# Optimization experiments

Measured on AMD Instinct MI355X. Metric: run time of the kernel, lower is better.

## Reference

```python
import jax, jax.numpy as jnp
import numpy as np

HIDDEN = 4096
N_HEADS = 32
QK_NOPE = 128
QK_ROPE = 64
QK_HEAD = QK_NOPE + QK_ROPE  # 192
V_HEAD = 128
Q_LORA = 1536
KV_LORA = 512
EPS = 1e-6
ROPE_BASE = 10000.0
T = 2048


def rmsnorm(x, g, eps=EPS):
    var = jnp.mean(x * x, axis=-1, keepdims=True)
    return x * jax.lax.rsqrt(var + eps) * g


def apply_rope_interleaved(x, cos, sin):
    # non-neox style: rotate interleaved pairs. x: [T, ..., d]; cos/sin: [T, d//2]
    x1 = x[..., 0::2]
    x2 = x[..., 1::2]
    while cos.ndim < x1.ndim:
        cos = cos[:, None]
        sin = sin[:, None]
    o1 = x1 * cos - x2 * sin
    o2 = x1 * sin + x2 * cos
    return jnp.stack([o1, o2], axis=-1).reshape(x.shape)


def setup_inputs() -> dict:
    key = jax.random.key(0)
    ks = jax.random.split(key, 8)
    s = lambda fan_in: 1.0 / np.sqrt(fan_in)
    return {
        "positions": jnp.arange(T, dtype=jnp.int32),
        "hidden_states": jax.random.normal(ks[0], (T, HIDDEN), jnp.float32),
        "wq_a": jax.random.normal(ks[1], (HIDDEN, Q_LORA), jnp.float32) * s(HIDDEN),
        "gq": jnp.ones((Q_LORA,), jnp.float32),
        "wq_b": jax.random.normal(ks[2], (Q_LORA, N_HEADS * QK_HEAD), jnp.float32) * s(Q_LORA),
        "wkv_a": jax.random.normal(ks[3], (HIDDEN, KV_LORA + QK_ROPE), jnp.float32) * s(HIDDEN),
        "gkv": jnp.ones((KV_LORA,), jnp.float32),
        "wkv_b": jax.random.normal(ks[4], (KV_LORA, N_HEADS * (QK_NOPE + V_HEAD)), jnp.float32) * s(KV_LORA),
        "wo": jax.random.normal(ks[5], (N_HEADS * V_HEAD, HIDDEN), jnp.float32) * s(N_HEADS * V_HEAD),
    }


def reference(positions, hidden_states, wq_a, gq, wq_b, wkv_a, gkv, wkv_b, wo):
    t = hidden_states.shape[0]
    scale = QK_HEAD ** -0.5

    # Q path: low-rank down-proj -> RMSNorm -> up-proj
    q = rmsnorm(hidden_states @ wq_a, gq) @ wq_b  # [T, H*192]
    q = q.reshape(t, N_HEADS, QK_HEAD)
    q_nope, q_pe = q[..., :QK_NOPE], q[..., QK_NOPE:]

    # KV path: compressed latent + decoupled rope key
    kv_a = hidden_states @ wkv_a  # [T, kv_lora + rope]
    c_kv, k_pe = kv_a[:, :KV_LORA], kv_a[:, KV_LORA:]
    kv = rmsnorm(c_kv, gkv) @ wkv_b  # [T, H*(nope+v)]
    kv = kv.reshape(t, N_HEADS, QK_NOPE + V_HEAD)
    k_nope, v = kv[..., :QK_NOPE], kv[..., QK_NOPE:]

    # RoPE (interleaved / non-neox)
    inv_freq = 1.0 / (ROPE_BASE ** (jnp.arange(0, QK_ROPE, 2, dtype=jnp.float32) / QK_ROPE))
    angles = positions.astype(jnp.float32)[:, None] * inv_freq[None, :]  # [T, rope/2]
    cos, sin = jnp.cos(angles), jnp.sin(angles)
    q_pe = apply_rope_interleaved(q_pe, cos, sin)          # [T, H, rope]
    k_pe = apply_rope_interleaved(k_pe, cos, sin)          # [T, rope]

    q_full = jnp.concatenate([q_nope, q_pe], axis=-1)       # [T, H, 192]
    k_full = jnp.concatenate(
        [k_nope, jnp.broadcast_to(k_pe[:, None, :], (t, N_HEADS, QK_ROPE))], axis=-1)

    scores = jnp.einsum('qhd,khd->hqk', q_full, k_full) * scale  # [H, T, T]
    causal = positions[:, None] >= positions[None, :]
    scores = jnp.where(causal[None], scores, jnp.finfo(scores.dtype).min)
    probs = jax.nn.softmax(scores, axis=-1)
    attn = jnp.einsum('hqk,khd->qhd', probs, v)              # [T, H, 128]
    return attn.reshape(t, N_HEADS * V_HEAD) @ wo            # [T, hidden]
```

## Files before the change

kernel.cpp:

```cpp
#include <hip/hip_runtime.h>
#include <hip/hip_bf16.h>
#include <stdint.h>

typedef __hip_bfloat16 bf16;
typedef unsigned short u16;
typedef short v8s __attribute__((ext_vector_type(8)));
typedef float v4f __attribute__((ext_vector_type(4)));

#define T_LEN   2048
#define HIDDEN  4096
#define N_HEADS 32
#define QK_NOPE 128
#define QK_ROPE 64
#define QK_HEAD 192
#define V_HEAD  128
#define Q_LORA  1536
#define KV_LORA 512
#define NFUSE   2176

enum { DT_BF16 = 0, DT_F32 = 1, DT_EXT = 2 };

__device__ __forceinline__ u16 f2b(float x) {
    union { bf16 h; u16 u; } cv; cv.h = __float2bfloat16(x); return cv.u;
}

typedef const __attribute__((address_space(1))) uint32_t* gas_ptr;
typedef __attribute__((address_space(3))) uint32_t* las_ptr;
__device__ __forceinline__ void gll16(const void* g, void* l) {
    __builtin_amdgcn_global_load_lds((gas_ptr)g, (las_ptr)l, 16, 0, 0);
}

__global__ __launch_bounds__(256) void convert_bf16(
    const void* __restrict__ X, u16* __restrict__ Y, int nelem,
    const uint32_t* __restrict__ probe)
{
    const bool f32 = (probe[0] & 0xFFFFu) == 0u;
    const int i = (blockIdx.x * 256 + threadIdx.x) * 8;
    if (i >= nelem) return;
    if (f32) {
        const float* x = (const float*)X + i;
        u16 o[8];
        #pragma unroll
        for (int e = 0; e < 8; ++e) o[e] = f2b(x[e]);
        *(uint4*)(Y + i) = *(const uint4*)o;
    } else {
        *(uint4*)(Y + i) = *(const uint4*)((const u16*)X + i);
    }
}

__global__ __launch_bounds__(256) void transpose_to_bf16(
    const void* __restrict__ W, u16* __restrict__ Wt,
    int K, int N, const uint32_t* __restrict__ probe)
{
    const bool f32 = (probe[0] & 0xFFFFu) == 0u;
    __shared__ uint32_t Ts[64 * 33];
    const int n0 = blockIdx.x * 64;
    const int k0 = blockIdx.y * 64;
    const int tid = threadIdx.x;
    {
        const int nc = (tid & 7) * 8;
        const int kp = tid >> 3;
        const int k = k0 + kp * 2;
        uint32_t vals[8];
        if (n0 >= N) {
            #pragma unroll
            for (int e = 0; e < 8; ++e) vals[e] = 0;
        } else if (f32) {
            const float* w0 = (const float*)W + (size_t)k * N + n0 + nc;
            const float* w1 = w0 + N;
            #pragma unroll
            for (int e = 0; e < 8; ++e)
                vals[e] = (uint32_t)f2b(w0[e]) | ((uint32_t)f2b(w1[e]) << 16);
        } else {
            const u16* w0 = (const u16*)W + (size_t)k * N + n0 + nc;
            const u16* w1 = w0 + N;
            u16 a[8], b[8];
            *(uint4*)a = *(const uint4*)w0;
            *(uint4*)b = *(const uint4*)w1;
            #pragma unroll
            for (int e = 0; e < 8; ++e)
                vals[e] = (uint32_t)a[e] | ((uint32_t)b[e] << 16);
        }
        #pragma unroll
        for (int e = 0; e < 8; ++e)
            Ts[(nc + e) * 33 + kp] = vals[e];
    }
    __syncthreads();
    {
        const int n = tid >> 2;
        const int kp0 = (tid & 3) * 8;
        u16 out[16];
        #pragma unroll
        for (int j = 0; j < 8; ++j) {
            const uint32_t v = Ts[n * 33 + kp0 + j];
            out[2 * j]     = (u16)(v & 0xFFFFu);
            out[2 * j + 1] = (u16)(v >> 16);
        }
        u16* dst = Wt + (size_t)(n0 + n) * K + k0 + kp0 * 2;
        *(uint4*)dst = *(const uint4*)out;
        *(uint4*)(dst + 8) = *(const uint4*)(out + 8);
    }
}

__global__ __launch_bounds__(256) void gemm_bt(
    const u16* __restrict__ A, const u16* __restrict__ Bt,
    void* __restrict__ C, int ccode,
    int N, int K, const uint32_t* __restrict__ probe)
{
    __shared__ __align__(16) u16 As[128 * 32];
    __shared__ __align__(16) u16 Bs[128 * 32];

    const int tid  = threadIdx.x;
    const int lane = tid & 63;
    const int wave = tid >> 6;
    const int quad = lane >> 4, l15 = lane & 15;
    const int wr = (wave >> 1) * 64, wc = (wave & 1) * 64;

    const int gx  = gridDim.x;
    const int nwg = gx * gridDim.y;
    int bid = blockIdx.y * gx + blockIdx.x;
    if ((nwg & 7) == 0)
        bid = (bid & 7) * (nwg >> 3) + (bid >> 3);
    const int bxl = bid % gx;
    const int byl = bid / gx;
    const size_t brow = (size_t)byl * 128;
    const size_t bcol = (size_t)bxl * 128;

    v4f acc[4][4];
    #pragma unroll
    for (int i = 0; i < 4; ++i)
        #pragma unroll
        for (int j = 0; j < 4; ++j)
            acc[i][j] = (v4f){0.f, 0.f, 0.f, 0.f};

    const int c0 = tid, c1 = tid + 256;
    const int r0 = c0 >> 2, e0 = (c0 & 3) * 8;
    const int r1 = c1 >> 2, e1 = (c1 & 3) * 8;
    const u16* Ab = A + brow * K;
    const u16* Bb = Bt + bcol * K;

    for (int k0 = 0; k0 < K; k0 += 32) {
        gll16(Ab + (size_t)r0 * K + k0 + e0, (void*)(As + c0 * 8));
        gll16(Ab + (size_t)r1 * K + k0 + e1, (void*)(As + c1 * 8));
        gll16(Bb + (size_t)r0 * K + k0 + e0, (void*)(Bs + c0 * 8));
        gll16(Bb + (size_t)r1 * K + k0 + e1, (void*)(Bs + c1 * 8));
        __syncthreads();

        v8s af[4], bf[4];
        #pragma unroll
        for (int i = 0; i < 4; ++i)
            af[i] = *(const v8s*)(As + (wr + i * 16 + l15) * 32 + quad * 8);
        #pragma unroll
        for (int j = 0; j < 4; ++j)
            bf[j] = *(const v8s*)(Bs + (wc + j * 16 + l15) * 32 + quad * 8);
        #pragma unroll
        for (int i = 0; i < 4; ++i)
            #pragma unroll
            for (int j = 0; j < 4; ++j)
                acc[i][j] = __builtin_amdgcn_mfma_f32_16x16x32_bf16(
                    af[i], bf[j], acc[i][j], 0, 0, 0);
        __syncthreads();
    }

    const bool c_f32 = (ccode == DT_F32) ||
                       (ccode == DT_EXT && (probe[0] & 0xFFFFu) == 0u);
    #pragma unroll
    for (int i = 0; i < 4; ++i) {
        #pragma unroll
        for (int r = 0; r < 4; ++r) {
            const size_t row = brow + wr + i * 16 + quad * 4 + r;
            #pragma unroll
            for (int j = 0; j < 4; ++j) {
                const size_t col = bcol + wc + j * 16 + l15;
                if (c_f32) ((float*)C)[row * N + col] = acc[i][j][r];
                else       ((u16*)C)[row * N + col]   = f2b(acc[i][j][r]);
            }
        }
    }
}

__global__ __launch_bounds__(256) void rmsnorm_kernel(
    const float* __restrict__ x, const void* __restrict__ g,
    bf16* __restrict__ y, int cols,
    const uint32_t* __restrict__ probe)
{
    const bool g_f32 = (probe[0] & 0xFFFFu) == 0u;
    const int row = blockIdx.x;
    const float* xr = x + (size_t)row * NFUSE;
    float ss = 0.f;
    for (int c = threadIdx.x; c < cols; c += 256) {
        float v = xr[c];
        ss += v * v;
    }
    #pragma unroll
    for (int off = 32; off > 0; off >>= 1) ss += __shfl_down(ss, off, 64);
    __shared__ float wsum[4];
    const int wave = threadIdx.x >> 6, lane = threadIdx.x & 63;
    if (lane == 0) wsum[wave] = ss;
    __syncthreads();
    const float tot = wsum[0] + wsum[1] + wsum[2] + wsum[3];
    const float inv = rsqrtf(tot / (float)cols + 1e-6f);
    for (int c = threadIdx.x; c < cols; c += 256) {
        const float gv = g_f32 ? ((const float*)g)[c]
                               : __bfloat162float(((const bf16*)g)[c]);
        y[(size_t)row * cols + c] = __float2bfloat16(xr[c] * inv * gv);
    }
}

__global__ void kpe_rope_kernel(const float* __restrict__ qkv,
                                const int* __restrict__ pos,
                                bf16* __restrict__ kpe)
{
    const int t = blockIdx.x;
    const int i = threadIdx.x;
    const float x1 = qkv[(size_t)t * NFUSE + 2048 + 2 * i];
    const float x2 = qkv[(size_t)t * NFUSE + 2048 + 2 * i + 1];
    const float inv_freq = powf(10000.f, -(float)(2 * i) / 64.f);
    const float ang = (float)pos[t] * inv_freq;
    float s, c;
    sincosf(ang, &s, &c);
    kpe[(size_t)t * 64 + 2 * i]     = __float2bfloat16(x1 * c - x2 * s);
    kpe[(size_t)t * 64 + 2 * i + 1] = __float2bfloat16(x1 * s + x2 * c);
}

__global__ __launch_bounds__(256) void qpe_rope_kernel(bf16* __restrict__ q,
                                                       const int* __restrict__ pos)
{
    const int idx = blockIdx.x * 256 + threadIdx.x;
    const int i = idx & 31;
    const int h = (idx >> 5) & 31;
    const int t = idx >> 10;
    if (t >= T_LEN) return;
    bf16* base = q + ((size_t)t * N_HEADS + h) * QK_HEAD + QK_NOPE + 2 * i;
    const float x1 = __bfloat162float(base[0]);
    const float x2 = __bfloat162float(base[1]);
    const float inv_freq = powf(10000.f, -(float)(2 * i) / 64.f);
    const float ang = (float)pos[t] * inv_freq;
    float s, c;
    sincosf(ang, &s, &c);
    base[0] = __float2bfloat16(x1 * c - x2 * s);
    base[1] = __float2bfloat16(x1 * s + x2 * c);
}

#define KS_LD 200
#define VT_LD 72
#define PS_LD 72

__global__ __launch_bounds__(256) void attn_mfma(
    const bf16* __restrict__ qg, const bf16* __restrict__ kvg,
    const bf16* __restrict__ kpeg, bf16* __restrict__ attng)
{
    __shared__ u16 Ks[64 * KS_LD];
    __shared__ u16 Vt[V_HEAD * VT_LD];
    __shared__ u16 Ps[4 * 32 * PS_LD];

    const int bx = blockIdx.x;
    const int h  = bx & 31;
    const int g  = bx >> 5;
    const int qt = (bx < 256) ? (15 - g) : (g - 8);
    const int q0 = qt * 128;
    const int nkt = 2 * qt + 2;

    const int tid  = threadIdx.x;
    const int wave = tid >> 6, lane = tid & 63;
    const int quad = lane >> 4, l15 = lane & 15;
    const float scale = 0.07216878364870323f;

    v8s qf[2][6];
    #pragma unroll
    for (int mi = 0; mi < 2; ++mi)
        #pragma unroll
        for (int ks = 0; ks < 6; ++ks)
            qf[mi][ks] = *(const v8s*)((const u16*)qg +
                (size_t)(q0 + wave * 32 + mi * 16 + l15) * 6144 +
                h * 192 + ks * 32 + quad * 8);

    v4f accO[2][8];
    #pragma unroll
    for (int mi = 0; mi < 2; ++mi)
        #pragma unroll
        for (int vs = 0; vs < 8; ++vs)
            accO[mi][vs] = (v4f){0.f, 0.f, 0.f, 0.f};
    float m_run[2][4], l_run[2][4];
    #pragma unroll
    for (int mi = 0; mi < 2; ++mi)
        #pragma unroll
        for (int r = 0; r < 4; ++r) { m_run[mi][r] = -1e30f; l_run[mi][r] = 0.f; }

    for (int kt = 0; kt < nkt; ++kt) {
        const int k0 = kt * 64;
        __syncthreads();
        {
            const int jj = tid >> 4;
            const int c0 = (tid & 15) * 16;
            #pragma unroll
            for (int p = 0; p < 4; ++p) {
                const int j = jj + p * 16;
                const u16* src = (const u16*)kvg +
                    (size_t)(k0 + j) * 8192 + h * 256 + c0;
                uint4 v0 = *(const uint4*)src;
                uint4 v1 = *(const uint4*)(src + 8);
                if (c0 < 128) {
                    u16* dst = &Ks[j * KS_LD + c0];
                    *(uint4*)dst = v0;
                    *(uint4*)(dst + 8) = v1;
                } else {
                    u16 buf[16];
                    *(uint4*)buf = v0;
                    *(uint4*)(buf + 8) = v1;
                    const int d0 = c0 - 128;
                    #pragma unroll
                    for (int e = 0; e < 16; ++e) {
                        const int d = d0 + e;
                        const int jswz = j ^ (((d >> 4) & 7) << 3);
                        Vt[d * VT_LD + jswz] = buf[e];
                    }
                }
            }
            const int j2 = tid >> 2;
            const int c2 = (tid & 3) * 16;
            const u16* src = (const u16*)kpeg + (size_t)(k0 + j2) * 64 + c2;
            uint4 w0 = *(const uint4*)src;
            uint4 w1 = *(const uint4*)(src + 8);
            u16* dst = &Ks[j2 * KS_LD + 128 + c2];
            *(uint4*)dst = w0;
            *(uint4*)(dst + 8) = w1;
        }
        __syncthreads();

        v4f accS[2][4];
        #pragma unroll
        for (int mi = 0; mi < 2; ++mi)
            #pragma unroll
            for (int nj = 0; nj < 4; ++nj)
                accS[mi][nj] = (v4f){0.f, 0.f, 0.f, 0.f};
        #pragma unroll
        for (int ks = 0; ks < 6; ++ks) {
            v8s kf[4];
            #pragma unroll
            for (int nj = 0; nj < 4; ++nj)
                kf[nj] = *(const v8s*)&Ks[(nj * 16 + l15) * KS_LD + ks * 32 + quad * 8];
            #pragma unroll
            for (int mi = 0; mi < 2; ++mi)
                #pragma unroll
                for (int nj = 0; nj < 4; ++nj)
                    accS[mi][nj] = __builtin_amdgcn_mfma_f32_16x16x32_bf16(
                        qf[mi][ks], kf[nj], accS[mi][nj], 0, 0, 0);
        }

        const bool need_mask = (kt >= 2 * qt);
        float p[2][4][4];
        float alpha[2][4];
        #pragma unroll
        for (int mi = 0; mi < 2; ++mi) {
            #pragma unroll
            for (int r = 0; r < 4; ++r) {
                const int qrow = q0 + wave * 32 + mi * 16 + quad * 4 + r;
                float sv[4];
                float rm = -1e30f;
                #pragma unroll
                for (int nj = 0; nj < 4; ++nj) {
                    float s = accS[mi][nj][r] * scale;
                    if (need_mask) {
                        const int jgl = k0 + nj * 16 + l15;
                        if (jgl > qrow) s = -1e30f;
                    }
                    sv[nj] = s;
                    rm = fmaxf(rm, s);
                }
                rm = fmaxf(rm, __shfl_xor(rm, 1));
                rm = fmaxf(rm, __shfl_xor(rm, 2));
                rm = fmaxf(rm, __shfl_xor(rm, 4));
                rm = fmaxf(rm, __shfl_xor(rm, 8));
                const float mo = m_run[mi][r];
                const float mn = fmaxf(mo, rm);
                const float al = __expf(mo - mn);
                float ps = 0.f;
                #pragma unroll
                for (int nj = 0; nj < 4; ++nj) {
                    const float pv = __expf(sv[nj] - mn);
                    p[mi][nj][r] = pv;
                    ps += pv;
                }
                ps += __shfl_xor(ps, 1);
                ps += __shfl_xor(ps, 2);
                ps += __shfl_xor(ps, 4);
                ps += __shfl_xor(ps, 8);
                l_run[mi][r] = l_run[mi][r] * al + ps;
                m_run[mi][r] = mn;
                alpha[mi][r] = al;
            }
        }

        #pragma unroll
        for (int mi = 0; mi < 2; ++mi)
            #pragma unroll
            for (int vs = 0; vs < 8; ++vs)
                #pragma unroll
                for (int r = 0; r < 4; ++r)
                    accO[mi][vs][r] *= alpha[mi][r];

        u16* psw = &Ps[wave * 32 * PS_LD];
        #pragma unroll
        for (int mi = 0; mi < 2; ++mi)
            #pragma unroll
            for (int nj = 0; nj < 4; ++nj)
                #pragma unroll
                for (int r = 0; r < 4; ++r)
                    psw[(mi * 16 + quad * 4 + r) * PS_LD + nj * 16 + l15] =
                        f2b(p[mi][nj][r]);

        #pragma unroll
        for (int kf = 0; kf < 2; ++kf) {
            v8s pf[2];
            #pragma unroll
            for (int mi = 0; mi < 2; ++mi)
                pf[mi] = *(const v8s*)&psw[(mi * 16 + l15) * PS_LD + kf * 32 + quad * 8];
            #pragma unroll
            for (int vs = 0; vs < 8; ++vs) {
                const int swz = (vs & 7) << 3;
                v8s vf = *(const v8s*)&Vt[(vs * 16 + l15) * VT_LD +
                                          ((kf * 32 + quad * 8) ^ swz)];
                #pragma unroll
                for (int mi = 0; mi < 2; ++mi)
                    accO[mi][vs] = __builtin_amdgcn_mfma_f32_16x16x32_bf16(
                        pf[mi], vf, accO[mi][vs], 0, 0, 0);
            }
        }
    }

    #pragma unroll
    for (int mi = 0; mi < 2; ++mi) {
        #pragma unroll
        for (int r = 0; r < 4; ++r) {
            const int qrow = q0 + wave * 32 + mi * 16 + quad * 4 + r;
            const float linv = 1.f / l_run[mi][r];
            #pragma unroll
            for (int vs = 0; vs < 8; ++vs)
                attng[(size_t)qrow * 4096 + h * 128 + vs * 16 + l15] =
                    __float2bfloat16(accO[mi][vs][r] * linv);
        }
    }
}

extern "C" void kernel_launch(void* const* d_in, const int* in_sizes, int n_in,
                              void* d_out, int out_size, void* d_ws, size_t ws_size,
                              hipStream_t stream)
{
    const int*  pos    = (const int*)d_in[0];
    const void* hidden = d_in[1];
    const void* wq_a   = d_in[2];
    const void* gq     = d_in[3];
    const void* wq_b   = d_in[4];
    const void* wkv_a  = d_in[5];
    const void* gkv    = d_in[6];
    const void* wkv_b  = d_in[7];
    const void* wo     = d_in[8];
    const uint32_t* probe = (const uint32_t*)gq;

    char* w = (char*)d_ws;
    u16*   h_bf   = (u16*)w;   w += (size_t)T_LEN * HIDDEN * 2;
    u16*   Wt_qkv = (u16*)w;   w += (size_t)NFUSE * HIDDEN * 2;
    u16*   Wt_qb  = (u16*)w;   w += (size_t)6144 * Q_LORA * 2;
    u16*   Wt_kvb = (u16*)w;   w += (size_t)8192 * KV_LORA * 2;
    u16*   Wt_o   = (u16*)w;   w += (size_t)HIDDEN * HIDDEN * 2;
    float* qkv    = (float*)w; w += (size_t)T_LEN * NFUSE * 4;
    u16*   q_norm = (u16*)w;   w += (size_t)T_LEN * Q_LORA * 2;
    u16*   q      = (u16*)w;   w += (size_t)T_LEN * N_HEADS * QK_HEAD * 2;
    u16*   ckv    = (u16*)w;   w += (size_t)T_LEN * KV_LORA * 2;
    u16*   kpe    = (u16*)w;   w += (size_t)T_LEN * QK_ROPE * 2;
    u16*   kv     = (u16*)w;   w += (size_t)T_LEN * N_HEADS * 256 * 2;
    u16*   attn   = Wt_qkv;

    convert_bf16<<<4096, 256, 0, stream>>>(hidden, h_bf, T_LEN * HIDDEN, probe);
    transpose_to_bf16<<<dim3(1536 / 64, HIDDEN / 64), 256, 0, stream>>>(
        wq_a, Wt_qkv, HIDDEN, 1536, probe);
    transpose_to_bf16<<<dim3(640 / 64, HIDDEN / 64), 256, 0, stream>>>(
        wkv_a, Wt_qkv + (size_t)1536 * HIDDEN, HIDDEN, 576, probe);
    transpose_to_bf16<<<dim3(6144 / 64, Q_LORA / 64), 256, 0, stream>>>(
        wq_b, Wt_qb, Q_LORA, 6144, probe);
    transpose_to_bf16<<<dim3(8192 / 64, KV_LORA / 64), 256, 0, stream>>>(
        wkv_b, Wt_kvb, KV_LORA, 8192, probe);
    transpose_to_bf16<<<dim3(HIDDEN / 64, HIDDEN / 64), 256, 0, stream>>>(
        wo, Wt_o, HIDDEN, HIDDEN, probe);

    gemm_bt<<<dim3(NFUSE / 128, T_LEN / 128), 256, 0, stream>>>(
        h_bf, Wt_qkv, qkv, DT_F32, NFUSE, HIDDEN, probe);

    rmsnorm_kernel<<<T_LEN, 256, 0, stream>>>(qkv, gq, (bf16*)q_norm, Q_LORA, probe);
    rmsnorm_kernel<<<T_LEN, 256, 0, stream>>>(qkv + 1536, gkv, (bf16*)ckv, KV_LORA, probe);
    kpe_rope_kernel<<<T_LEN, 32, 0, stream>>>(qkv, pos, (bf16*)kpe);

    gemm_bt<<<dim3(6144 / 128, T_LEN / 128), 256, 0, stream>>>(
        q_norm, Wt_qb, q, DT_BF16, 6144, Q_LORA, probe);
    qpe_rope_kernel<<<(T_LEN * N_HEADS * 32) / 256, 256, 0, stream>>>((bf16*)q, pos);

    gemm_bt<<<dim3(8192 / 128, T_LEN / 128), 256, 0, stream>>>(
        ckv, Wt_kvb, kv, DT_BF16, 8192, KV_LORA, probe);

    attn_mfma<<<dim3(N_HEADS * (T_LEN / 128)), 256, 0, stream>>>(
        (const bf16*)q, (const bf16*)kv, (const bf16*)kpe, (bf16*)attn);

    gemm_bt<<<dim3(HIDDEN / 128, T_LEN / 128), 256, 0, stream>>>(
        attn, Wt_o, d_out, DT_EXT, HIDDEN, HIDDEN, probe);
}
```

Baseline: 778.2 us.

## Split attention block into 8 waves of 16 query rows each

The attention kernel now uses 512 threads (8 waves), each owning 16 query rows instead of 32. This halves per-wave accumulator and Q-fragment registers and doubles waves per block to raise occupancy and latency hiding. K/V tile loading is spread across more threads. The block ordering is also simplified to a plain descending query-tile order, dropping the previous interleaved schedule. In exchange, each wave reuses every K/V LDS fragment for fewer MFMAs.

```diff
diff --git a/kernel.cpp b/kernel.cpp
--- a/kernel.cpp
+++ b/kernel.cpp
@@ -246,18 +246,17 @@
 #define VT_LD 72
 #define PS_LD 72
 
-__global__ __launch_bounds__(256) void attn_mfma(
+__global__ __launch_bounds__(512, 4) void attn_mfma(
     const bf16* __restrict__ qg, const bf16* __restrict__ kvg,
     const bf16* __restrict__ kpeg, bf16* __restrict__ attng)
 {
     __shared__ u16 Ks[64 * KS_LD];
     __shared__ u16 Vt[V_HEAD * VT_LD];
-    __shared__ u16 Ps[4 * 32 * PS_LD];
+    __shared__ u16 Ps[8 * 16 * PS_LD];
 
     const int bx = blockIdx.x;
     const int h  = bx & 31;
-    const int g  = bx >> 5;
-    const int qt = (bx < 256) ? (15 - g) : (g - 8);
+    const int qt = 15 - (bx >> 5);
     const int q0 = qt * 128;
     const int nkt = 2 * qt + 2;
 
@@ -266,26 +265,20 @@
     const int quad = lane >> 4, l15 = lane & 15;
     const float scale = 0.07216878364870323f;
 
-    v8s qf[2][6];
-    #pragma unroll
-    for (int mi = 0; mi < 2; ++mi)
-        #pragma unroll
-        for (int ks = 0; ks < 6; ++ks)
-            qf[mi][ks] = *(const v8s*)((const u16*)qg +
-                (size_t)(q0 + wave * 32 + mi * 16 + l15) * 6144 +
-                h * 192 + ks * 32 + quad * 8);
-
-    v4f accO[2][8];
-    #pragma unroll
-    for (int mi = 0; mi < 2; ++mi)
-        #pragma unroll
-        for (int vs = 0; vs < 8; ++vs)
-            accO[mi][vs] = (v4f){0.f, 0.f, 0.f, 0.f};
-    float m_run[2][4], l_run[2][4];
-    #pragma unroll
-    for (int mi = 0; mi < 2; ++mi)
-        #pragma unroll
-        for (int r = 0; r < 4; ++r) { m_run[mi][r] = -1e30f; l_run[mi][r] = 0.f; }
+    v8s qf[6];
+    #pragma unroll
+    for (int ks = 0; ks < 6; ++ks)
+        qf[ks] = *(const v8s*)((const u16*)qg +
+            (size_t)(q0 + wave * 16 + l15) * 6144 +
+            h * 192 + ks * 32 + quad * 8);
+
+    v4f accO[8];
+    #pragma unroll
+    for (int vs = 0; vs < 8; ++vs)
+        accO[vs] = (v4f){0.f, 0.f, 0.f, 0.f};
+    float m_run[4], l_run[4];
+    #pragma unroll
+    for (int r = 0; r < 4; ++r) { m_run[r] = -1e30f; l_run[r] = 0.f; }
 
     for (int kt = 0; kt < nkt; ++kt) {
         const int k0 = kt * 64;
@@ -294,8 +287,8 @@
             const int jj = tid >> 4;
             const int c0 = (tid & 15) * 16;
             #pragma unroll
-            for (int p = 0; p < 4; ++p) {
-                const int j = jj + p * 16;
+            for (int p = 0; p < 2; ++p) {
+                const int j = jj + p * 32;
                 const u16* src = (const u16*)kvg +
                     (size_t)(k0 + j) * 8192 + h * 256 + c0;
                 uint4 v0 = *(const uint4*)src;
@@ -317,23 +310,19 @@
                     }
                 }
             }
-            const int j2 = tid >> 2;
-            const int c2 = (tid & 3) * 16;
+            const int j2 = tid >> 3;
+            const int c2 = (tid & 7) * 8;
             const u16* src = (const u16*)kpeg + (size_t)(k0 + j2) * 64 + c2;
             uint4 w0 = *(const uint4*)src;
-            uint4 w1 = *(const uint4*)(src + 8);
             u16* dst = &Ks[j2 * KS_LD + 128 + c2];
             *(uint4*)dst = w0;
-            *(uint4*)(dst + 8) = w1;
         }
         __syncthreads();
 
-        v4f accS[2][4];
-        #pragma unroll
-        for (int mi = 0; mi < 2; ++mi)
-            #pragma unroll
-            for (int nj = 0; nj < 4; ++nj)
-                accS[mi][nj] = (v4f){0.f, 0.f, 0.f, 0.f};
+        v4f accS[4];
+        #pragma unroll
+        for (int nj = 0; nj < 4; ++nj)
+            accS[nj] = (v4f){0.f, 0.f, 0.f, 0.f};
         #pragma unroll
         for (int ks = 0; ks < 6; ++ks) {
             v8s kf[4];
@@ -341,105 +330,87 @@
             for (int nj = 0; nj < 4; ++nj)
                 kf[nj] = *(const v8s*)&Ks[(nj * 16 + l15) * KS_LD + ks * 32 + quad * 8];
             #pragma unroll
-            for (int mi = 0; mi < 2; ++mi)
-                #pragma unroll
-                for (int nj = 0; nj < 4; ++nj)
-                    accS[mi][nj] = __builtin_amdgcn_mfma_f32_16x16x32_bf16(
-                        qf[mi][ks], kf[nj], accS[mi][nj], 0, 0, 0);
+            for (int nj = 0; nj < 4; ++nj)
+                accS[nj] = __builtin_amdgcn_mfma_f32_16x16x32_bf16(
+                    qf[ks], kf[nj], accS[nj], 0, 0, 0);
         }
 
         const bool need_mask = (kt >= 2 * qt);
-        float p[2][4][4];
-        float alpha[2][4];
-        #pragma unroll
-        for (int mi = 0; mi < 2; ++mi) {
-            #pragma unroll
-            for (int r = 0; r < 4; ++r) {
-                const int qrow = q0 + wave * 32 + mi * 16 + quad * 4 + r;
-                float sv[4];
-                float rm = -1e30f;
-                #pragma unroll
-                for (int nj = 0; nj < 4; ++nj) {
-                    float s = accS[mi][nj][r] * scale;
-                    if (need_mask) {
-                        const int jgl = k0 + nj * 16 + l15;
-                        if (jgl > qrow) s = -1e30f;
-                    }
-                    sv[nj] = s;
-                    rm = fmaxf(rm, s);
+        float p[4][4];
+        float alpha[4];
+        #pragma unroll
+        for (int r = 0; r < 4; ++r) {
+            const int qrow = q0 + wave * 16 + quad * 4 + r;
+            float sv[4];
+            float rm = -1e30f;
+            #pragma unroll
+            for (int nj = 0; nj < 4; ++nj) {
+                float s = accS[nj][r] * scale;
+                if (need_mask) {
+                    const int jgl = k0 + nj * 16 + l15;
+                    if (jgl > qrow) s = -1e30f;
                 }
-                rm = fmaxf(rm, __shfl_xor(rm, 1));
-                rm = fmaxf(rm, __shfl_xor(rm, 2));
-                rm = fmaxf(rm, __shfl_xor(rm, 4));
-                rm = fmaxf(rm, __shfl_xor(rm, 8));
-                const float mo = m_run[mi][r];
-                const float mn = fmaxf(mo, rm);
-                const float al = __expf(mo - mn);
-                float ps = 0.f;
-                #pragma unroll
-                for (int nj = 0; nj < 4; ++nj) {
-                    const float pv = __expf(sv[nj] - mn);
-                    p[mi][nj][r] = pv;
-                    ps += pv;
-                }
-                ps += __shfl_xor(ps, 1);
-                ps += __shfl_xor(ps, 2);
-                ps += __shfl_xor(ps, 4);
-                ps += __shfl_xor(ps, 8);
-                l_run[mi][r] = l_run[mi][r] * al + ps;
-                m_run[mi][r] = mn;
-                alpha[mi][r] = al;
+                sv[nj] = s;
+                rm = fmaxf(rm, s);
             }
-        }
-
-        #pragma unroll
-        for (int mi = 0; mi < 2; ++mi)
-            #pragma unroll
-            for (int vs = 0; vs < 8; ++vs)
-                #pragma unroll
-                for (int r = 0; r < 4; ++r)
-                    accO[mi][vs][r] *= alpha[mi][r];
-
-        u16* psw = &Ps[wave * 32 * PS_LD];
-        #pragma unroll
-        for (int mi = 0; mi < 2; ++mi)
-            #pragma unroll
-            for (int nj = 0; nj < 4; ++nj)
-                #pragma unroll
-                for (int r = 0; r < 4; ++r)
-                    psw[(mi * 16 + quad * 4 + r) * PS_LD + nj * 16 + l15] =
-                        f2b(p[mi][nj][r]);
+            rm = fmaxf(rm, __shfl_xor(rm, 1));
+            rm = fmaxf(rm, __shfl_xor(rm, 2));
+            rm = fmaxf(rm, __shfl_xor(rm, 4));
+            rm = fmaxf(rm, __shfl_xor(rm, 8));
+            const float mo = m_run[r];
+            const float mn = fmaxf(mo, rm);
+            const float al = __expf(mo - mn);
+            float ps = 0.f;
+            #pragma unroll
+            for (int nj = 0; nj < 4; ++nj) {
+                const float pv = __expf(sv[nj] - mn);
+                p[nj][r] = pv;
+                ps += pv;
+            }
+            ps += __shfl_xor(ps, 1);
+            ps += __shfl_xor(ps, 2);
+            ps += __shfl_xor(ps, 4);
+            ps += __shfl_xor(ps, 8);
+            l_run[r] = l_run[r] * al + ps;
+            m_run[r] = mn;
+            alpha[r] = al;
+        }
+
+        #pragma unroll
+        for (int vs = 0; vs < 8; ++vs)
+            #pragma unroll
+            for (int r = 0; r < 4; ++r)
+                accO[vs][r] *= alpha[r];
+
+        u16* psw = &Ps[wave * 16 * PS_LD];
+        #pragma unroll
+        for (int nj = 0; nj < 4; ++nj)
+            #pragma unroll
+            for (int r = 0; r < 4; ++r)
+                psw[(quad * 4 + r) * PS_LD + nj * 16 + l15] = f2b(p[nj][r]);
 
         #pragma unroll
         for (int kf = 0; kf < 2; ++kf) {
-            v8s pf[2];
-            #pragma unroll
-            for (int mi = 0; mi < 2; ++mi)
-                pf[mi] = *(const v8s*)&psw[(mi * 16 + l15) * PS_LD + kf * 32 + quad * 8];
+            v8s pf = *(const v8s*)&psw[l15 * PS_LD + kf * 32 + quad * 8];
             #pragma unroll
             for (int vs = 0; vs < 8; ++vs) {
                 const int swz = (vs & 7) << 3;
                 v8s vf = *(const v8s*)&Vt[(vs * 16 + l15) * VT_LD +
                                           ((kf * 32 + quad * 8) ^ swz)];
-                #pragma unroll
-                for (int mi = 0; mi < 2; ++mi)
-                    accO[mi][vs] = __builtin_amdgcn_mfma_f32_16x16x32_bf16(
-                        pf[mi], vf, accO[mi][vs], 0, 0, 0);
+                accO[vs] = __builtin_amdgcn_mfma_f32_16x16x32_bf16(
+                    pf, vf, accO[vs], 0, 0, 0);
             }
         }
     }
 
     #pragma unroll
-    for (int mi = 0; mi < 2; ++mi) {
-        #pragma unroll
-        for (int r = 0; r < 4; ++r) {
-            const int qrow = q0 + wave * 32 + mi * 16 + quad * 4 + r;
-            const float linv = 1.f / l_run[mi][r];
-            #pragma unroll
-            for (int vs = 0; vs < 8; ++vs)
-                attng[(size_t)qrow * 4096 + h * 128 + vs * 16 + l15] =
-                    __float2bfloat16(accO[mi][vs][r] * linv);
-        }
+    for (int r = 0; r < 4; ++r) {
+        const int qrow = q0 + wave * 16 + quad * 4 + r;
+        const float linv = 1.f / l_run[r];
+        #pragma unroll
+        for (int vs = 0; vs < 8; ++vs)
+            attng[(size_t)qrow * 4096 + h * 128 + vs * 16 + l15] =
+                __float2bfloat16(accO[vs][r] * linv);
     }
 }
 
@@ -498,7 +469,7 @@
     gemm_bt<<<dim3(8192 / 128, T_LEN / 128), 256, 0, stream>>>(
         ckv, Wt_kvb, kv, DT_BF16, 8192, KV_LORA, probe);
 
-    attn_mfma<<<dim3(N_HEADS * (T_LEN / 128)), 256, 0, stream>>>(
+    attn_mfma<<<dim3(N_HEADS * (T_LEN / 128)), 512, 0, stream>>>(
         (const bf16*)q, (const bf16*)kv, (const bf16*)kpe, (bf16*)attn);
 
     gemm_bt<<<dim3(HIDDEN / 128, T_LEN / 128), 256, 0, stream>>>(
```

Result: slower. 825.7 us (+6.1%).
